# Performance work log

Hardware: AMD Instinct MI355X
Metric: run time of the kernel (lower is better)

The kernel has to match this reference:

```python
import jax, jax.numpy as jnp
import numpy as np

HEADS = 8
DIM_HEAD = 64
DIM = 128
TOPK = (8, 8, 8)  # depth, height, width


def chan_ln(x, g, b):
    # channel layernorm over axis=1 (biased variance), eps added to std
    mean = jnp.mean(x, axis=1, keepdims=True)
    var = jnp.var(x, axis=1, keepdims=True)
    return g * (x - mean) / (jnp.sqrt(var) + 1e-6) + b


def l2norm(x):
    # F.normalize(dim=1): divide by max(||x||_2, eps)
    n = jnp.sqrt(jnp.sum(x * x, axis=1, keepdims=True))
    return x / jnp.maximum(n, 1e-12)


def _forward(query_source, context, w_q, w_kv, w_out,
             ctx_gamma, ctx_beta, qs_gamma, qs_beta, out_gamma, out_beta, gamma):
    b, c, Dq, Hq, Wq = query_source.shape
    Dc, Hc, Wc = context.shape[2:]
    kd, kh, kw = TOPK

    ctx = chan_ln(context, ctx_gamma, ctx_beta)
    qs = chan_ln(query_source, qs_gamma, qs_beta)

    # 1x1x1 convs == channel matmuls
    kv = jnp.einsum('bcdhw,oc->bodhw', ctx, w_kv)   # (b, 2*inner, D, H, W)
    k, v = jnp.split(kv, 2, axis=1)
    q = jnp.einsum('bcdhw,oc->bodhw', qs, w_q)      # (b, inner, D, H, W)

    def fold(t):  # (b, h*c, D,H,W) -> (b*h, c, D,H,W)
        return t.reshape(b * HEADS, DIM_HEAD, *t.shape[2:])

    q, k, v = fold(q), fold(k), fold(v)
    q, k = l2norm(q), l2norm(k)

    q_probe = jnp.sum(q, axis=(2, 3, 4))            # (bh, c)
    k_abs = jnp.abs(k)

    if kd < Dc:
        score = jnp.einsum('bc,bcd->bd', q_probe, jnp.sum(k_abs, axis=(3, 4)))
        idx = jax.lax.top_k(score, kd)[1][:, None, :, None, None]
        k = jnp.take_along_axis(k, idx, axis=2)
        v = jnp.take_along_axis(v, idx, axis=2)
    if kh < Hc:
        score = jnp.einsum('bc,bch->bh', q_probe, jnp.sum(k_abs, axis=(2, 4)))
        idx = jax.lax.top_k(score, kh)[1][:, None, None, :, None]
        k = jnp.take_along_axis(k, idx, axis=3)
        v = jnp.take_along_axis(v, idx, axis=3)
    if kw < Wc:
        score = jnp.einsum('bc,bcw->bw', q_probe, jnp.sum(k_abs, axis=(2, 3)))
        idx = jax.lax.top_k(score, kw)[1][:, None, None, None, :]
        k = jnp.take_along_axis(k, idx, axis=4)
        v = jnp.take_along_axis(v, idx, axis=4)

    def flat(t):  # (bh, c, d, h, w) -> (bh, d*h*w, c)
        return t.reshape(t.shape[0], t.shape[1], -1).transpose(0, 2, 1)

    qf, kf, vf = flat(q), flat(k), flat(v)
    sim = jnp.einsum('bic,bjc->bij', qf, kf)        # (bh, Nq, Nkv)
    attn = jax.nn.softmax(sim, axis=-1)
    out = jnp.einsum('bij,bjc->bic', attn, vf)      # (bh, Nq, c)

    out = out.reshape(b, HEADS, Dq, Hq, Wq, DIM_HEAD)
    out = out.transpose(0, 1, 5, 2, 3, 4).reshape(b, HEADS * DIM_HEAD, Dq, Hq, Wq)
    out = jnp.einsum('bcdhw,oc->bodhw', out, w_out)
    out = chan_ln(out, out_gamma, out_beta)
    return gamma * out + query_source


def setup_inputs() -> dict:
    key = jax.random.key(0)
    ks = jax.random.split(key, 6)
    b, c, D, H, W = 2, DIM, 16, 32, 32
    inner = HEADS * DIM_HEAD
    ones = jnp.ones((1, c, 1, 1, 1), jnp.float32)
    zeros = jnp.zeros((1, c, 1, 1, 1), jnp.float32)
    return {
        'query_source': jax.random.normal(ks[0], (b, c, D, H, W), jnp.float32),
        'context': jax.random.normal(ks[1], (b, c, D, H, W), jnp.float32),
        'w_q': jax.random.normal(ks[2], (inner, c), jnp.float32) / np.sqrt(c).astype(np.float32),
        'w_kv': jax.random.normal(ks[3], (2 * inner, c), jnp.float32) / np.sqrt(c).astype(np.float32),
        'w_out': jax.random.normal(ks[4], (c, inner), jnp.float32) / np.sqrt(inner).astype(np.float32),
        'ctx_gamma': ones, 'ctx_beta': zeros,
        'qs_gamma': ones, 'qs_beta': zeros,
        'out_gamma': ones, 'out_beta': zeros,
        'gamma': jnp.full((1,), 0.5, jnp.float32),
    }


def reference(query_source, context, w_q, w_kv, w_out,
              ctx_gamma, ctx_beta, qs_gamma, qs_beta, out_gamma, out_beta, gamma):
    return _forward(query_source, context, w_q, w_kv, w_out,
                    ctx_gamma, ctx_beta, qs_gamma, qs_beta, out_gamma, out_beta, gamma)
```

## Files before the change

kernel.cpp:

```cpp
#include <hip/hip_runtime.h>
#include <hip/hip_bf16.h>

#define S_SP 16384
#define NKV 512

typedef short short8 __attribute__((ext_vector_type(8)));
typedef float v4f   __attribute__((ext_vector_type(4)));

__device__ __forceinline__ unsigned short f2bf(float x){
  union { float f; unsigned u; } v; v.f = x;
  unsigned r = v.u + 0x7FFFu + ((v.u >> 16) & 1u);
  return (unsigned short)(r >> 16);
}
__device__ __forceinline__ float bf2f(unsigned short h){
  union { unsigned u; float f; } v; v.u = ((unsigned)h) << 16; return v.f;
}

#if defined(__has_builtin)
#if __has_builtin(__builtin_amdgcn_cvt_pk_bf16_f32)
#define HAVE_PKBF 1
#endif
#endif

__device__ __forceinline__ unsigned pk2(float a, float b){
#ifdef HAVE_PKBF
  typedef __bf16 bf16x2 __attribute__((ext_vector_type(2)));
  union { bf16x2 v; unsigned u; } r;
  r.v = __builtin_amdgcn_cvt_pk_bf16_f32(a, b);
  return r.u;
#else
  return (unsigned)f2bf(a) | ((unsigned)f2bf(b) << 16);
#endif
}

__device__ __forceinline__ short8 u2s8(uint4 u){
  union { uint4 u; short8 s; } x; x.u = u; return x.s;
}

__global__ __launch_bounds__(256) void k_stats(const float* __restrict__ ctx,
                                               const float* __restrict__ qs,
                                               const float* __restrict__ ctx_g,
                                               const float* __restrict__ ctx_b,
                                               const float* __restrict__ qs_g,
                                               const float* __restrict__ qs_b,
                                               const float* __restrict__ wq,
                                               const float* __restrict__ wkv,
                                               float* __restrict__ MEAN,
                                               float* __restrict__ INV,
                                               unsigned short* __restrict__ XTC_hi,
                                               unsigned short* __restrict__ XTC_lo,
                                               unsigned short* __restrict__ XTQ_hi,
                                               unsigned short* __restrict__ XTQ_lo,
                                               unsigned short* __restrict__ WQh,
                                               unsigned short* __restrict__ WQl,
                                               unsigned short* __restrict__ WKh,
                                               unsigned short* __restrict__ WKl){
  __shared__ float r1[4][64];
  __shared__ float r2[4][64];
  __shared__ float mb[64], ib[64];
  __shared__ __align__(16) unsigned short TH[64*136];
  __shared__ __align__(16) unsigned short TL[64*136];
  int bx = blockIdx.x;
  int t = threadIdx.x;
  if (bx >= 1024){
    int wb = bx - 1024;
    int isK = wb >> 5;
    size_t i8 = ((size_t)(wb & 31)*256 + t)*8;
    const float* srcw = isK ? wkv : wq;
    unsigned short* dh = isK ? WKh : WQh;
    unsigned short* dl = isK ? WKl : WQl;
    v4f a  = *(const v4f*)(srcw + i8);
    v4f b2 = *(const v4f*)(srcw + i8 + 4);
    unsigned short h[8], l[8];
    #pragma unroll
    for (int i=0;i<4;i++){
      h[i]   = f2bf(a[i]);  l[i]   = f2bf(a[i]  - bf2f(h[i]));
      h[i+4] = f2bf(b2[i]); l[i+4] = f2bf(b2[i] - bf2f(h[i+4]));
    }
    uint4 uh, ul;
    uh.x = (unsigned)h[0] | ((unsigned)h[1]<<16);
    uh.y = (unsigned)h[2] | ((unsigned)h[3]<<16);
    uh.z = (unsigned)h[4] | ((unsigned)h[5]<<16);
    uh.w = (unsigned)h[6] | ((unsigned)h[7]<<16);
    ul.x = (unsigned)l[0] | ((unsigned)l[1]<<16);
    ul.y = (unsigned)l[2] | ((unsigned)l[3]<<16);
    ul.z = (unsigned)l[4] | ((unsigned)l[5]<<16);
    ul.w = (unsigned)l[6] | ((unsigned)l[7]<<16);
    *(uint4*)(dh + i8) = uh;
    *(uint4*)(dl + i8) = ul;
    return;
  }
  int tt = bx >> 9; int b = (bx >> 8) & 1; int sc = bx & 255;
  int sv = t & 63, cg = t >> 6;
  int s = sc*64 + sv;
  const float* src = (tt ? qs : ctx) + ((size_t)b*128 + cg*32)*S_SP + s;
  const float* G  = tt ? qs_g : ctx_g;
  const float* Bv = tt ? qs_b : ctx_b;
  float xv[32];
  float sum = 0.f, ss = 0.f;
  #pragma unroll
  for (int c = 0; c < 32; c++){
    float v = src[(size_t)c*S_SP];
    xv[c] = v;
    sum += v; ss += v*v;
  }
  r1[cg][sv] = sum; r2[cg][sv] = ss;
  __syncthreads();
  if (t < 64){
    float sm = r1[0][t]+r1[1][t]+r1[2][t]+r1[3][t];
    float sq = r2[0][t]+r2[1][t]+r2[2][t]+r2[3][t];
    float mean = sm * 0.0078125f;
    float var  = fmaxf(sq * 0.0078125f - mean*mean, 0.f);
    float inv  = 1.f/(sqrtf(var) + 1e-6f);
    int o = tt*2*S_SP + b*S_SP + sc*64 + t;
    MEAN[o] = mean; INV[o] = inv;
    mb[t] = mean; ib[t] = inv;
  }
  __syncthreads();
  float m = mb[sv], iv = ib[sv];
  #pragma unroll
  for (int i = 0; i < 32; i += 2){
    int c = cg*32 + i;
    float y0 = G[c]  *(xv[i]  -m)*iv + Bv[c];
    float y1 = G[c+1]*(xv[i+1]-m)*iv + Bv[c+1];
    unsigned short h0 = f2bf(y0), h1 = f2bf(y1);
    unsigned short l0 = f2bf(y0 - bf2f(h0)), l1 = f2bf(y1 - bf2f(h1));
    *(unsigned*)&TH[sv*136 + c] = (unsigned)h0 | ((unsigned)h1 << 16);
    *(unsigned*)&TL[sv*136 + c] = (unsigned)l0 | ((unsigned)l1 << 16);
  }
  __syncthreads();
  int row = t >> 2, seg = (t & 3) * 32;
  unsigned short* XH = tt ? XTQ_hi : XTC_hi;
  unsigned short* XL = tt ? XTQ_lo : XTC_lo;
  size_t go = ((size_t)b*S_SP + sc*64 + row)*128 + seg;
  #pragma unroll
  for (int k2 = 0; k2 < 4; k2++){
    *(uint4*)(XH + go + k2*8) = *(const uint4*)&TH[row*136 + seg + k2*8];
    *(uint4*)(XL + go + k2*8) = *(const uint4*)&TL[row*136 + seg + k2*8];
  }
}

template<int ISK>
__global__ __launch_bounds__(256, 2) void k_proj(
    const unsigned short* __restrict__ XH, const unsigned short* __restrict__ XL,
    const unsigned short* __restrict__ WH, const unsigned short* __restrict__ WL,
    unsigned short* __restrict__ QBF, float* __restrict__ QP,
    float* __restrict__ SCORE){
  __shared__ float qpl[128];
  __shared__ float qacc[128];
  __shared__ float wacc[64];
  int bx = blockIdx.x;
  int og = bx >> 7, b = (bx >> 6) & 1, stile = bx & 63;
  int t = threadIdx.x, wvi = t >> 6, lane = t & 63;
  int quad = lane >> 4, l15 = lane & 15;
  int sw0 = stile*256 + wvi*64;
  int bh0 = b*8 + og*2;
  if (ISK){
    if (t < 128) qpl[t] = QP[bh0*64 + t];
    if (t < 64) wacc[t] = 0.f;
    __syncthreads();
  } else {
    if (t < 128) qacc[t] = 0.f;
  }
  v4f acc[8][4];
  #pragma unroll
  for (int i=0;i<8;i++)
    #pragma unroll
    for (int j=0;j<4;j++) acc[i][j] = (v4f){0.f,0.f,0.f,0.f};
  size_t wrow = ((size_t)(og*128 + l15))*128 + quad*8;
  size_t xrow = ((size_t)b*S_SP + sw0 + l15)*128 + quad*8;
  #pragma unroll 1
  for (int ks=0; ks<4; ks++){
    int ko = ks*32;
    uint4 bhv[4], blv[4], av[8];
    #pragma unroll
    for (int nt=0;nt<4;nt++){
      bhv[nt] = *(const uint4*)(XH + xrow + nt*2048 + ko);
      blv[nt] = *(const uint4*)(XL + xrow + nt*2048 + ko);
    }
    #pragma unroll
    for (int mt=0;mt<8;mt++) av[mt] = *(const uint4*)(WH + wrow + mt*2048 + ko);
    #pragma unroll
    for (int mt=0;mt<8;mt++){
      short8 am = u2s8(av[mt]);
      #pragma unroll
      for (int nt=0;nt<4;nt++)
        acc[mt][nt] = __builtin_amdgcn_mfma_f32_16x16x32_bf16(am, u2s8(bhv[nt]), acc[mt][nt], 0, 0, 0);
      #pragma unroll
      for (int nt=0;nt<4;nt++)
        acc[mt][nt] = __builtin_amdgcn_mfma_f32_16x16x32_bf16(am, u2s8(blv[nt]), acc[mt][nt], 0, 0, 0);
    }
    #pragma unroll
    for (int mt=0;mt<8;mt++){
      short8 am = u2s8(*(const uint4*)(WL + wrow + mt*2048 + ko));
      #pragma unroll
      for (int nt=0;nt<4;nt++)
        acc[mt][nt] = __builtin_amdgcn_mfma_f32_16x16x32_bf16(am, u2s8(bhv[nt]), acc[mt][nt], 0, 0, 0);
    }
  }
  float inv0[4], inv1[4];
  #pragma unroll
  for (int nt=0;nt<4;nt++){
    float p0 = 0.f, p1 = 0.f;
    #pragma unroll
    for (int mt=0;mt<4;mt++)
      #pragma unroll
      for (int r=0;r<4;r++){
        p0 += acc[mt][nt][r]*acc[mt][nt][r];
        p1 += acc[mt+4][nt][r]*acc[mt+4][nt][r];
      }
    p0 += __shfl_xor(p0,16,64); p0 += __shfl_xor(p0,32,64);
    p1 += __shfl_xor(p1,16,64); p1 += __shfl_xor(p1,32,64);
    inv0[nt] = 1.f/fmaxf(sqrtf(p0),1e-12f);
    inv1[nt] = 1.f/fmaxf(sqrtf(p1),1e-12f);
  }
  if (!ISK){
    #pragma unroll
    for (int mt=0;mt<8;mt++)
      #pragma unroll
      for (int nt=0;nt<4;nt++){
        float iv = (mt<4) ? inv0[nt] : inv1[nt];
        #pragma unroll
        for (int r=0;r<4;r++) acc[mt][nt][r] *= iv;
      }
    #pragma unroll
    for (int mt=0;mt<8;mt++){
      int bh = bh0 + (mt>>2);
      #pragma unroll
      for (int nt=0;nt<4;nt++){
        int s = sw0 + nt*16 + l15;
        uint2 wv;
        wv.x = pk2(acc[mt][nt][0], acc[mt][nt][1]);
        wv.y = pk2(acc[mt][nt][2], acc[mt][nt][3]);
        *(uint2*)(QBF + ((size_t)bh*S_SP + s)*64 + (mt&3)*16 + quad*4) = wv;
      }
    }
    __syncthreads();
    #pragma unroll
    for (int mt=0;mt<8;mt++){
      #pragma unroll
      for (int r=0;r<4;r++){
        float v = acc[mt][0][r]+acc[mt][1][r]+acc[mt][2][r]+acc[mt][3][r];
        v += __shfl_xor(v,1,64); v += __shfl_xor(v,2,64);
        v += __shfl_xor(v,4,64); v += __shfl_xor(v,8,64);
        if (l15 == 0)
          atomicAdd(&qacc[(mt>>2)*64 + (mt&3)*16 + quad*4 + r], v);
      }
    }
    __syncthreads();
    if (t < 128) atomicAdd(QP + bh0*64 + t, qacc[t]);
  } else {
    float v0[4] = {0,0,0,0}, v1[4] = {0,0,0,0};
    #pragma unroll
    for (int mt=0;mt<8;mt++){
      #pragma unroll
      for (int r=0;r<4;r++){
        float w = qpl[mt*16 + quad*4 + r];
        #pragma unroll
        for (int nt=0;nt<4;nt++){
          float av = fabsf(acc[mt][nt][r]) * w;
          if (mt < 4) v0[nt] += av; else v1[nt] += av;
        }
      }
    }
    #pragma unroll
    for (int nt=0;nt<4;nt++){
      v0[nt] += __shfl_xor(v0[nt],16,64); v0[nt] += __shfl_xor(v0[nt],32,64);
      v1[nt] += __shfl_xor(v1[nt],16,64); v1[nt] += __shfl_xor(v1[nt],32,64);
      v0[nt] *= inv0[nt]; v1[nt] *= inv1[nt];
    }
    float w00 = v0[0]+v0[2], w10 = v0[1]+v0[3];
    float w01 = v1[0]+v1[2], w11 = v1[1]+v1[3];
    float h00 = v0[0]+v0[1], h01 = v0[2]+v0[3];
    float h10 = v1[0]+v1[1], h11 = v1[2]+v1[3];
    #pragma unroll
    for (int mm=1; mm<16; mm<<=1){
      h00 += __shfl_xor(h00,mm,64); h01 += __shfl_xor(h01,mm,64);
      h10 += __shfl_xor(h10,mm,64); h11 += __shfl_xor(h11,mm,64);
    }
    if (lane < 16){
      atomicAdd(&wacc[l15],      w00);
      atomicAdd(&wacc[16+l15],   w10);
      atomicAdd(&wacc[32+l15],   w01);
      atomicAdd(&wacc[48+l15],   w11);
    }
    if (lane == 0){
      int hb = 16 + (stile&3)*8 + wvi*2;
      atomicAdd(SCORE + bh0*80 + hb,     h00);
      atomicAdd(SCORE + bh0*80 + hb + 1, h01);
      atomicAdd(SCORE + (bh0+1)*80 + hb,     h10);
      atomicAdd(SCORE + (bh0+1)*80 + hb + 1, h11);
      atomicAdd(SCORE + bh0*80 + (stile>>2), h00+h01);
      atomicAdd(SCORE + (bh0+1)*80 + (stile>>2), h10+h11);
    }
    __syncthreads();
    if (t < 64) atomicAdd(SCORE + (bh0 + (t>>5))*80 + 48 + (t&31), wacc[t]);
  }
}

__global__ __launch_bounds__(256) void k_gather(const float* __restrict__ ctx,
    const float* __restrict__ wkv, const float* __restrict__ ctx_g,
    const float* __restrict__ ctx_b, const float* __restrict__ MEAN,
    const float* __restrict__ INV, const float* __restrict__ SCORE,
    unsigned short* __restrict__ KG, unsigned short* __restrict__ VGT){
  __shared__ float wlds[64*129];
  __shared__ float xln[32*128];
  __shared__ float scb[80];
  __shared__ int sidx[24];
  int bx = blockIdx.x;
  int bh = bx >> 5, jc = (bx >> 1) & 15, type = bx & 1;
  int head = bh & 7, b = bh >> 3;
  int t = threadIdx.x;
  if (t < 80) scb[t] = SCORE[bh*80 + t];
  {
    int oc = t>>2, ks = (t&3)*32;
    const float* wr = wkv + ((size_t)(type*512 + head*64 + oc))*128 + ks;
    #pragma unroll 8
    for (int i=0;i<32;i++) wlds[oc*129 + ks + i] = wr[i];
  }
  __syncthreads();
  if (t < 64){
    #pragma unroll 1
    for (int a=0;a<3;a++){
      int n = a ? 32 : 16;
      int off = (a==0) ? 0 : (a==1 ? 16 : 48);
      float v = (t < n) ? scb[off+t] : -3.4e38f;
      #pragma unroll 1
      for (int it=0; it<8; it++){
        float bv = v; int bi = t;
        #pragma unroll
        for (int mm=1; mm<32; mm<<=1){
          float ov = __shfl_xor(bv, mm, 64);
          int oi = __shfl_xor(bi, mm, 64);
          if (ov > bv || (ov == bv && oi < bi)){ bv = ov; bi = oi; }
        }
        if (t == bi) v = -3.4e38f;
        if (t == 0) sidx[a*8+it] = bi;
      }
    }
  }
  __syncthreads();
  {
    int jl = t>>3, seg = (t&7)*16;
    int jj = jc*32 + jl;
    int dsel = sidx[jj>>6], hsel = sidx[8 + ((jj>>3)&7)], wsel = sidx[16 + (jj&7)];
    int sj = dsel*1024 + hsel*32 + wsel;
    float mn = MEAN[b*S_SP + sj];
    float iv = INV[b*S_SP + sj];
    #pragma unroll
    for (int i=0;i<16;i++){
      int cc = seg + i;
      float raw = ctx[((size_t)(b*128 + cc))*S_SP + sj];
      xln[jl*128 + cc] = ctx_g[cc]*(raw - mn)*iv + ctx_b[cc];
    }
  }
  __syncthreads();
  int c = t & 63, jg = t >> 6;
  float accv[8] = {};
  #pragma unroll 4
  for (int k=0;k<128;k++){
    float wv = wlds[c*129 + k];
    #pragma unroll
    for (int m=0;m<8;m++) accv[m] += wv * xln[(jg + 4*m)*128 + k];
  }
  #pragma unroll
  for (int m=0;m<8;m++){
    int jj = jc*32 + jg + 4*m;
    float a = accv[m];
    if (type == 0){
      float sq = a*a;
      #pragma unroll
      for (int mm=32; mm; mm>>=1) sq += __shfl_xor(sq, mm, 64);
      float rn = 1.f/fmaxf(sqrtf(sq), 1e-12f);
      KG[((size_t)bh*NKV + jj)*64 + c] = f2bf(a*rn);
    } else {
      VGT[((size_t)bh*64 + c)*NKV + jj] = f2bf(a);
    }
  }
}

__global__ __launch_bounds__(256) void k_attn(const unsigned short* __restrict__ QBF,
    const unsigned short* __restrict__ KG, const unsigned short* __restrict__ VGT,
    unsigned short* __restrict__ AOUT){
  __shared__ __align__(16) unsigned short kst[128*64];
  __shared__ __align__(16) unsigned short vst[64*128];
  __shared__ __align__(16) unsigned short pst[4][64*32];
  int bx = blockIdx.x;
  int bh = bx >> 6, qb = bx & 63;
  int t = threadIdx.x;
  int wvi = t >> 6, lane = t & 63;
  int quad = lane >> 4, l15 = lane & 15;
  int q0 = qb*256 + wvi*64;
  const unsigned short* kgb = KG + (size_t)bh*NKV*64;
  const unsigned short* vgb = VGT + (size_t)bh*64*NKV;
  short8 bq[4][2];
  #pragma unroll
  for (int qt=0; qt<4; qt++){
    const unsigned short* qp_ = QBF + ((size_t)bh*S_SP + q0 + qt*16 + l15)*64 + quad*8;
    union { uint4 u; short8 s; } u0, u1;
    u0.u = *(const uint4*)(qp_);
    u1.u = *(const uint4*)(qp_ + 32);
    bq[qt][0] = u0.s; bq[qt][1] = u1.s;
  }
  v4f oacc[4][4];
  #pragma unroll
  for (int i=0;i<4;i++)
    #pragma unroll
    for (int j=0;j<4;j++) oacc[i][j] = (v4f){0.f,0.f,0.f,0.f};
  float lsum[4] = {0.f,0.f,0.f,0.f};
  unsigned short* pw = pst[wvi];
  for (int ch=0; ch<4; ch++){
    __syncthreads();
    {
      int jl = t>>1, bb = (t&1)*4;
      const unsigned short* sp = kgb + (size_t)(ch*128 + jl)*64 + (t&1)*32;
      unsigned short* dp = kst + jl*64;
      int sw = jl & 7;
      #pragma unroll
      for (int i=0;i<4;i++) *(uint4*)(dp + (((bb+i)^sw)*8)) = *(const uint4*)(sp + i*8);
    }
    {
      int cc = t>>2, bb = (t&3)*4;
      const unsigned short* sp = vgb + (size_t)cc*NKV + ch*128 + (t&3)*32;
      unsigned short* dp = vst + cc*128;
      int sw = cc & 7;
      #pragma unroll
      for (int i=0;i<4;i++) *(uint4*)(dp + (((bb+i)^sw)*8)) = *(const uint4*)(sp + i*8);
    }
    __syncthreads();
    #pragma unroll
    for (int sub=0; sub<4; sub++){
      v4f s[2][4];
      #pragma unroll
      for (int j2=0; j2<2; j2++){
        int jr = (sub*2 + j2)*16 + l15;
        const unsigned short* kr = kst + jr*64;
        int sk = jr & 7;
        union { uint4 u; short8 s; } a0, a1;
        a0.u = *(const uint4*)(kr + ((quad^sk)*8));
        a1.u = *(const uint4*)(kr + (((quad+4)^sk)*8));
        __builtin_amdgcn_s_setprio(1);
        #pragma unroll
        for (int qt=0; qt<4; qt++){
          v4f z = {0.f,0.f,0.f,0.f};
          z = __builtin_amdgcn_mfma_f32_16x16x32_bf16(a0.s, bq[qt][0], z, 0, 0, 0);
          z = __builtin_amdgcn_mfma_f32_16x16x32_bf16(a1.s, bq[qt][1], z, 0, 0, 0);
          s[j2][qt] = z;
        }
        __builtin_amdgcn_s_setprio(0);
      }
      #pragma unroll
      for (int j2=0; j2<2; j2++){
        #pragma unroll
        for (int qt=0; qt<4; qt++){
          v4f p;
          #pragma unroll
          for (int r=0;r<4;r++) p[r] = __expf(s[j2][qt][r] - 1.0f);
          lsum[qt] += p[0]+p[1]+p[2]+p[3];
          uint2 wv;
          wv.x = pk2(p[0], p[1]);
          wv.y = pk2(p[2], p[3]);
          int qr = qt*16 + l15;
          *(uint2*)&pw[qr*32 + (((j2*2+(quad>>1))^(qr&3))*8) + (quad&1)*4] = wv;
        }
      }
      short8 bp[4];
      #pragma unroll
      for (int qt=0; qt<4; qt++){
        int qr = qt*16 + l15;
        union { uint4 u; short8 s; } ub;
        ub.u = *(const uint4*)&pw[qr*32 + ((quad^(qr&3))*8)];
        bp[qt] = ub.s;
      }
      #pragma unroll
      for (int ct=0; ct<4; ct++){
        int cr = ct*16 + l15;
        union { uint4 u; short8 s; } av;
        av.u = *(const uint4*)&vst[cr*128 + (((sub*4+quad)^(cr&7))*8)];
        __builtin_amdgcn_s_setprio(1);
        #pragma unroll
        for (int qt=0; qt<4; qt++)
          oacc[ct][qt] = __builtin_amdgcn_mfma_f32_16x16x32_bf16(av.s, bp[qt], oacc[ct][qt], 0, 0, 0);
        __builtin_amdgcn_s_setprio(0);
      }
    }
  }
  float rl[4];
  #pragma unroll
  for (int qt=0; qt<4; qt++){
    float l = lsum[qt];
    l += __shfl_xor(l, 16, 64);
    l += __shfl_xor(l, 32, 64);
    rl[qt] = 1.f/l;
  }
  #pragma unroll
  for (int qt=0; qt<4; qt++){
    #pragma unroll
    for (int ct=0; ct<4; ct++){
      v4f o = oacc[ct][qt];
      uint2 wv;
      wv.x = pk2(o[0]*rl[qt], o[1]*rl[qt]);
      wv.y = pk2(o[2]*rl[qt], o[3]*rl[qt]);
      *(uint2*)(AOUT + ((size_t)bh*S_SP + q0 + qt*16 + l15)*64 + ct*16 + quad*4) = wv;
    }
  }
}

__global__ __launch_bounds__(256) void k_out(const unsigned short* __restrict__ AOUT,
    const float* __restrict__ wout, const float* __restrict__ out_g,
    const float* __restrict__ out_b, const float* __restrict__ gamma,
    const float* __restrict__ qsrc, float* __restrict__ OUT){
  __shared__ __align__(16) unsigned short wl[128*40];
  __shared__ float lnp[4][2][64];
  __shared__ float mbuf[64], sbuf[64], ogl[128], obl[128];
  int bx = blockIdx.x; int b = bx>>8; int stile = bx&255; int s0 = stile*64;
  int t = threadIdx.x; int w = t>>6; int lane = t&63;
  int q = lane>>4; int l15 = lane&15;
  if (t < 128){ ogl[t] = out_g[t]; obl[t] = out_b[t]; }
  v4f acc[2][4];
  #pragma unroll
  for (int i=0;i<2;i++)
    #pragma unroll
    for (int j=0;j<4;j++) acc[i][j] = (v4f){0.f,0.f,0.f,0.f};
  for (int kt=0; kt<16; kt++){
    __syncthreads();
    {
      int c = t>>1, kb = (t&1)*16;
      const float* wr = wout + (size_t)c*512 + kt*32 + kb;
      v4f a0 = *(const v4f*)wr, a1 = *(const v4f*)(wr+4);
      v4f a2 = *(const v4f*)(wr+8), a3 = *(const v4f*)(wr+12);
      uint4 u0, u1;
      u0.x = pk2(a0[0], a0[1]); u0.y = pk2(a0[2], a0[3]);
      u0.z = pk2(a1[0], a1[1]); u0.w = pk2(a1[2], a1[3]);
      u1.x = pk2(a2[0], a2[1]); u1.y = pk2(a2[2], a2[3]);
      u1.z = pk2(a3[0], a3[1]); u1.w = pk2(a3[2], a3[3]);
      *(uint4*)&wl[c*40+kb]   = u0;
      *(uint4*)&wl[c*40+kb+8] = u1;
    }
    __syncthreads();
    short8 af[2];
    #pragma unroll
    for (int mt=0;mt<2;mt++){
      union { uint4 u; short8 s; } ua;
      ua.u = *(const uint4*)&wl[(w*32+mt*16+l15)*40 + q*8];
      af[mt] = ua.s;
    }
    int head = kt>>1; int cc0 = (kt&1)*32 + q*8;
    const unsigned short* bp = AOUT + ((size_t)((b*8+head)*S_SP + s0 + l15))*64 + cc0;
    #pragma unroll
    for (int nt=0;nt<4;nt++){
      union { uint4 u; short8 s; } ub;
      ub.u = *(const uint4*)(bp + (size_t)nt*16*64);
      #pragma unroll
      for (int mt=0;mt<2;mt++)
        acc[mt][nt] = __builtin_amdgcn_mfma_f32_16x16x32_bf16(af[mt], ub.s, acc[mt][nt], 0, 0, 0);
    }
  }
  #pragma unroll
  for (int nt=0;nt<4;nt++){
    float p1 = 0.f, p2 = 0.f;
    #pragma unroll
    for (int mt=0;mt<2;mt++)
      #pragma unroll
      for (int r=0;r<4;r++){ float v = acc[mt][nt][r]; p1 += v; p2 += v*v; }
    p1 += __shfl_xor(p1,16,64); p1 += __shfl_xor(p1,32,64);
    p2 += __shfl_xor(p2,16,64); p2 += __shfl_xor(p2,32,64);
    if (q == 0){ lnp[w][0][nt*16+l15] = p1; lnp[w][1][nt*16+l15] = p2; }
  }
  __syncthreads();
  if (t < 64){
    float m = (lnp[0][0][t]+lnp[1][0][t]+lnp[2][0][t]+lnp[3][0][t]) * 0.0078125f;
    float qq = (lnp[0][1][t]+lnp[1][1][t]+lnp[2][1][t]+lnp[3][1][t]) * 0.0078125f;
    float var = fmaxf(qq - m*m, 0.f);
    mbuf[t] = m;
    sbuf[t] = 1.f/(sqrtf(var) + 1e-6f);
  }
  __syncthreads();
  float gs = gamma[0];
  #pragma unroll
  for (int nt=0;nt<4;nt++){
    int sl = nt*16 + l15;
    float mm = mbuf[sl], ssc = sbuf[sl];
    #pragma unroll
    for (int mt=0;mt<2;mt++){
      #pragma unroll
      for (int r=0;r<4;r++){
        int c = w*32 + mt*16 + q*4 + r;
        size_t adr = ((size_t)(b*128+c))*S_SP + s0 + sl;
        float yn = (acc[mt][nt][r]-mm)*ssc;
        OUT[adr] = gs*(ogl[c]*yn + obl[c]) + qsrc[adr];
      }
    }
  }
}

extern "C" void kernel_launch(void* const* d_in, const int* in_sizes, int n_in,
                              void* d_out, int out_size, void* d_ws, size_t ws_size,
                              hipStream_t stream){
  const float* qsrc  = (const float*)d_in[0];
  const float* ctx   = (const float*)d_in[1];
  const float* wq    = (const float*)d_in[2];
  const float* wkv   = (const float*)d_in[3];
  const float* wout  = (const float*)d_in[4];
  const float* ctx_g = (const float*)d_in[5];
  const float* ctx_b = (const float*)d_in[6];
  const float* qs_g  = (const float*)d_in[7];
  const float* qs_b  = (const float*)d_in[8];
  const float* out_g = (const float*)d_in[9];
  const float* out_b = (const float*)d_in[10];
  const float* gamma = (const float*)d_in[11];
  float* OUT = (float*)d_out;
  char* ws = (char*)d_ws;
  float* QP    = (float*)(ws);
  float* SCORE = (float*)(ws + 4096);
  float* MEAN  = (float*)(ws + 16384);
  float* INV   = (float*)(ws + 278528);
  unsigned short* QBF  = (unsigned short*)(ws + 544768);
  unsigned short* KG   = (unsigned short*)(ws + 34099200);
  unsigned short* VGT  = (unsigned short*)(ws + 35147776);
  unsigned short* AOUT = (unsigned short*)(ws + 36196352);
  unsigned short* WQh = (unsigned short*)(ws + 34099200);
  unsigned short* WQl = (unsigned short*)(ws + 34230272);
  unsigned short* WKh = (unsigned short*)(ws + 34361344);
  unsigned short* WKl = (unsigned short*)(ws + 34492416);
  unsigned short* XTQh = (unsigned short*)(ws + 36196352);
  unsigned short* XTQl = (unsigned short*)(ws + 44584960);
  unsigned short* XTCh = (unsigned short*)(ws + 52973568);
  unsigned short* XTCl = (unsigned short*)(ws + 61362176);

  hipMemsetAsync(ws, 0, 9216, stream);
  k_stats<<<1088, 256, 0, stream>>>(ctx, qsrc, ctx_g, ctx_b, qs_g, qs_b, wq, wkv,
                                    MEAN, INV, XTCh, XTCl, XTQh, XTQl,
                                    WQh, WQl, WKh, WKl);
  k_proj<0><<<512, 256, 0, stream>>>(XTQh, XTQl, WQh, WQl, QBF, QP, SCORE);
  k_proj<1><<<512, 256, 0, stream>>>(XTCh, XTCl, WKh, WKl, QBF, QP, SCORE);
  k_gather<<<512, 256, 0, stream>>>(ctx, wkv, ctx_g, ctx_b, MEAN, INV, SCORE, KG, VGT);
  k_attn<<<1024, 256, 0, stream>>>(QBF, KG, VGT, AOUT);
  k_out<<<512, 256, 0, stream>>>(AOUT, wout, out_g, out_b, gamma, qsrc, OUT);
}
```

Measured before the change: 300.2 us.

## Load K/V MFMA operands directly from global memory, drop LDS staging

The attention kernel no longer stages K and V chunks through shared memory with block-wide barriers. Each wave now reads its MFMA operand fragments straight from global memory (relying on L1/L2 reuse across waves), the P scratch buffer uses padded rows instead of an XOR swizzle, and launch bounds request 4 blocks per CU. This removes the __syncthreads pairs and LDS footprint to raise occupancy and cut barrier stalls. The cost is redundant global loads across the four waves and higher load latency exposed inside the MFMA loop.

```diff
diff --git a/kernel.cpp b/kernel.cpp
--- a/kernel.cpp
+++ b/kernel.cpp
@@ -379,12 +379,10 @@
   }
 }
 
-__global__ __launch_bounds__(256) void k_attn(const unsigned short* __restrict__ QBF,
+__global__ __launch_bounds__(256, 4) void k_attn(const unsigned short* __restrict__ QBF,
     const unsigned short* __restrict__ KG, const unsigned short* __restrict__ VGT,
     unsigned short* __restrict__ AOUT){
-  __shared__ __align__(16) unsigned short kst[128*64];
-  __shared__ __align__(16) unsigned short vst[64*128];
-  __shared__ __align__(16) unsigned short pst[4][64*32];
+  __shared__ __align__(16) unsigned short pst[4][64*40];
   int bx = blockIdx.x;
   int bh = bx >> 6, qb = bx & 63;
   int t = threadIdx.x;
@@ -409,74 +407,52 @@
     for (int j=0;j<4;j++) oacc[i][j] = (v4f){0.f,0.f,0.f,0.f};
   float lsum[4] = {0.f,0.f,0.f,0.f};
   unsigned short* pw = pst[wvi];
+  const unsigned short* krb = kgb + (size_t)l15*64 + quad*8;
+  const unsigned short* vrb = vgb + (size_t)(l15)*NKV + quad*8;
+  #pragma unroll 1
   for (int ch=0; ch<4; ch++){
-    __syncthreads();
-    {
-      int jl = t>>1, bb = (t&1)*4;
-      const unsigned short* sp = kgb + (size_t)(ch*128 + jl)*64 + (t&1)*32;
-      unsigned short* dp = kst + jl*64;
-      int sw = jl & 7;
-      #pragma unroll
-      for (int i=0;i<4;i++) *(uint4*)(dp + (((bb+i)^sw)*8)) = *(const uint4*)(sp + i*8);
-    }
-    {
-      int cc = t>>2, bb = (t&3)*4;
-      const unsigned short* sp = vgb + (size_t)cc*NKV + ch*128 + (t&3)*32;
-      unsigned short* dp = vst + cc*128;
-      int sw = cc & 7;
-      #pragma unroll
-      for (int i=0;i<4;i++) *(uint4*)(dp + (((bb+i)^sw)*8)) = *(const uint4*)(sp + i*8);
-    }
-    __syncthreads();
     #pragma unroll
     for (int sub=0; sub<4; sub++){
-      v4f s[2][4];
       #pragma unroll
       for (int j2=0; j2<2; j2++){
-        int jr = (sub*2 + j2)*16 + l15;
-        const unsigned short* kr = kst + jr*64;
-        int sk = jr & 7;
+        int jt = (sub*2 + j2)*16;
+        const unsigned short* kr = krb + (size_t)(ch*128 + jt)*64;
         union { uint4 u; short8 s; } a0, a1;
-        a0.u = *(const uint4*)(kr + ((quad^sk)*8));
-        a1.u = *(const uint4*)(kr + (((quad+4)^sk)*8));
+        a0.u = *(const uint4*)(kr);
+        a1.u = *(const uint4*)(kr + 32);
+        v4f s4[4];
         __builtin_amdgcn_s_setprio(1);
         #pragma unroll
         for (int qt=0; qt<4; qt++){
           v4f z = {0.f,0.f,0.f,0.f};
           z = __builtin_amdgcn_mfma_f32_16x16x32_bf16(a0.s, bq[qt][0], z, 0, 0, 0);
           z = __builtin_amdgcn_mfma_f32_16x16x32_bf16(a1.s, bq[qt][1], z, 0, 0, 0);
-          s[j2][qt] = z;
+          s4[qt] = z;
         }
         __builtin_amdgcn_s_setprio(0);
-      }
-      #pragma unroll
-      for (int j2=0; j2<2; j2++){
         #pragma unroll
         for (int qt=0; qt<4; qt++){
           v4f p;
           #pragma unroll
-          for (int r=0;r<4;r++) p[r] = __expf(s[j2][qt][r] - 1.0f);
+          for (int r=0;r<4;r++) p[r] = __expf(s4[qt][r] - 1.0f);
           lsum[qt] += p[0]+p[1]+p[2]+p[3];
           uint2 wv;
           wv.x = pk2(p[0], p[1]);
           wv.y = pk2(p[2], p[3]);
-          int qr = qt*16 + l15;
-          *(uint2*)&pw[qr*32 + (((j2*2+(quad>>1))^(qr&3))*8) + (quad&1)*4] = wv;
+          *(uint2*)&pw[(qt*16 + l15)*40 + j2*16 + quad*4] = wv;
         }
       }
       short8 bp[4];
       #pragma unroll
       for (int qt=0; qt<4; qt++){
-        int qr = qt*16 + l15;
         union { uint4 u; short8 s; } ub;
-        ub.u = *(const uint4*)&pw[qr*32 + ((quad^(qr&3))*8)];
+        ub.u = *(const uint4*)&pw[(qt*16 + l15)*40 + quad*8];
         bp[qt] = ub.s;
       }
       #pragma unroll
       for (int ct=0; ct<4; ct++){
-        int cr = ct*16 + l15;
         union { uint4 u; short8 s; } av;
-        av.u = *(const uint4*)&vst[cr*128 + (((sub*4+quad)^(cr&7))*8)];
+        av.u = *(const uint4*)(vrb + (size_t)ct*16*NKV + ch*128 + sub*32);
         __builtin_amdgcn_s_setprio(1);
         #pragma unroll
         for (int qt=0; qt<4; qt++)
```

Result: slower. 790.3 us (+163.3%).
